# Optimization experiments

Measured on AMD Instinct MI355X. Metric: run time of the kernel, lower is better.

## Reference

```python
import jax, jax.numpy as jnp
import numpy as np

EPS_COS = 1e-8   # F.cosine_similarity eps
EPS_CLAMP = 1e-6 # torch.clamp min on similarities


def setup_inputs() -> dict:
    key = jax.random.key(0)
    k1, = jax.random.split(key, 1)
    N, G, D = 2048, 10, 512
    x = jax.random.normal(k1, (N, G, D), dtype=jnp.float32)
    w = jnp.asarray(10.0, dtype=jnp.float32)  # learnable scale (init_w)
    b = jnp.asarray(-5.0, dtype=jnp.float32)  # learnable bias (init_b)
    return {"x": x, "w": w, "b": b}


def _safe_norm(v, axis=-1, keepdims=True):
    return jnp.maximum(jnp.linalg.norm(v, axis=axis, keepdims=keepdims), EPS_COS)


def reference(x, w, b):
    # x: [N, G, D]  (N speakers, G utterances each, D-dim embeddings)
    N, G, D = x.shape
    sum_x = jnp.sum(x, axis=1)                    # [N, D]
    centroids = sum_x / G                         # [N, D] full centroids
    # exclusion centroid for utterance g of speaker n: mean over the other G-1
    exc = (sum_x[:, None, :] - x) / (G - 1)       # [N, G, D]

    # diagonal: cos(x[n,g], exc_centroid[n,g])
    diag = jnp.sum(x * exc, axis=-1) / (
        _safe_norm(x, keepdims=False) * _safe_norm(exc, keepdims=False)
    )                                             # [N, G]

    # off-diagonal: cos(x[n,g], centroids[m]) for all m
    xn = x / _safe_norm(x)                        # [N, G, D]
    cn = centroids / _safe_norm(centroids)        # [N, D]
    sim = jnp.einsum("ngd,md->ngm", xn, cn)       # [N, G, N]

    # replace m == n entries with the excluded-centroid similarity
    eye = jnp.eye(N, dtype=bool)                  # [N, N]
    sim = jnp.where(eye[:, None, :], diag[:, :, None], sim)
    sim = jnp.maximum(sim, EPS_CLAMP)

    logits = sim * w + b                          # [N, G, N]
    logp = jax.nn.log_softmax(logits, axis=-1)
    n_idx = jnp.arange(N)
    # CE with label = speaker index n, repeated over the G utterances
    nloss = -jnp.mean(logp[n_idx[:, None], jnp.arange(G)[None, :], n_idx[:, None]])

    pred = jnp.argmax(logits, axis=-1)            # [N, G]
    prec1 = jnp.mean((pred == n_idx[:, None]).astype(jnp.float32)) * 100.0
    return nloss, prec1
```

## Files before the change

kernel.cpp:

```cpp
#include <hip/hip_runtime.h>
#include <math.h>

#define NSPK 2048
#define GUT  10
#define DIM  512
#define NG   (NSPK*GUT)

#define BM 256
#define BN 128
#define BK 64
#define NCB (NSPK/BN)
#define NHB (NCB*2)
#define NRB (NG/BM)
#define NKC (DIM/BK)
#define K3B (NG/256)
#define LBUF 24576

typedef __attribute__((ext_vector_type(4))) int int4v;

__device__ inline void gload_lds16(const void* g, void* l) {
  __builtin_amdgcn_global_load_lds(
      (const __attribute__((address_space(1))) void*)g,
      (__attribute__((address_space(3))) void*)l, 16, 0, 0);
}

__device__ __forceinline__ float mergesum(float a, float b, int mask, bool bsel) {
  const float ss = bsel ? a : b;
  const float sk = bsel ? b : a;
  return sk + __shfl_xor(ss, mask);
}
__device__ inline unsigned pack4i8(float a, float b, float c, float d, float qs) {
  const int q0 = (int)rintf(a * qs) & 255, q1 = (int)rintf(b * qs) & 255;
  const int q2 = (int)rintf(c * qs) & 255, q3 = (int)rintf(d * qs) & 255;
  return (unsigned)q0 | ((unsigned)q1 << 8) | ((unsigned)q2 << 16) | ((unsigned)q3 << 24);
}

__global__ __launch_bounds__(256) void k1_prep(const float* __restrict__ x,
    unsigned char* __restrict__ xn8, unsigned char* __restrict__ cn8,
    float* __restrict__ xs, float* __restrict__ cs, float* __restrict__ diag)
{
  const int n = blockIdx.x * 4 + (threadIdx.x >> 6);
  const int l = threadIdx.x & 63;
  const float* xb = x + (size_t)n * GUT * DIM + l * 8;

  float4 xa[GUT], xc[GUT];
#pragma unroll
  for (int g = 0; g < GUT; ++g) {
    xa[g] = *reinterpret_cast<const float4*>(xb + g * DIM);
    xc[g] = *reinterpret_cast<const float4*>(xb + g * DIM + 4);
  }
  float s0=0,s1=0,s2=0,s3=0,s4=0,s5=0,s6=0,s7=0;
#pragma unroll
  for (int g = 0; g < GUT; ++g) {
    s0 += xa[g].x; s1 += xa[g].y; s2 += xa[g].z; s3 += xa[g].w;
    s4 += xc[g].x; s5 += xc[g].y; s6 += xc[g].z; s7 += xc[g].w;
  }
  float P[GUT], D[GUT];
  float mxa = 0.f;
#pragma unroll
  for (int g = 0; g < GUT; ++g) {
    P[g] = xa[g].x*xa[g].x + xa[g].y*xa[g].y + xa[g].z*xa[g].z + xa[g].w*xa[g].w
         + xc[g].x*xc[g].x + xc[g].y*xc[g].y + xc[g].z*xc[g].z + xc[g].w*xc[g].w;
    D[g] = xa[g].x*s0 + xa[g].y*s1 + xa[g].z*s2 + xa[g].w*s3
         + xc[g].x*s4 + xc[g].y*s5 + xc[g].z*s6 + xc[g].w*s7;
    const float m1 = fmaxf(fmaxf(fabsf(xa[g].x), fabsf(xa[g].y)), fmaxf(fabsf(xa[g].z), fabsf(xa[g].w)));
    const float m2 = fmaxf(fmaxf(fabsf(xc[g].x), fabsf(xc[g].y)), fmaxf(fabsf(xc[g].z), fabsf(xc[g].w)));
    mxa = fmaxf(mxa, fmaxf(m1, m2));
  }
  float S = s0*s0+s1*s1+s2*s2+s3*s3+s4*s4+s5*s5+s6*s6+s7*s7;
  float ms = fmaxf(fmaxf(fmaxf(fabsf(s0),fabsf(s1)),fmaxf(fabsf(s2),fabsf(s3))),
                   fmaxf(fmaxf(fabsf(s4),fabsf(s5)),fmaxf(fabsf(s6),fabsf(s7))));

  const bool b0 = l & 1, b1 = l & 2, b2 = l & 4, b3 = l & 8, b4 = l & 16;
  float P01 = mergesum(P[0], P[1], 1, b0);
  float P23 = mergesum(P[2], P[3], 1, b0);
  float P45 = mergesum(P[4], P[5], 1, b0);
  float P67 = mergesum(P[6], P[7], 1, b0);
  float P89 = mergesum(P[8], P[9], 1, b0);
  float D01 = mergesum(D[0], D[1], 1, b0);
  float D23 = mergesum(D[2], D[3], 1, b0);
  float D45 = mergesum(D[4], D[5], 1, b0);
  float D67 = mergesum(D[6], D[7], 1, b0);
  float D89 = mergesum(D[8], D[9], 1, b0);
  S += __shfl_xor(S, 1);
  float PA1 = mergesum(P01, P23, 2, b1);
  float PB1 = mergesum(P45, P67, 2, b1);
  float DA1 = mergesum(D01, D23, 2, b1);
  float DB1 = mergesum(D45, D67, 2, b1);
  P89 += __shfl_xor(P89, 2); D89 += __shfl_xor(D89, 2); S += __shfl_xor(S, 2);
  float PA = mergesum(PA1, PB1, 4, b2);
  float DA = mergesum(DA1, DB1, 4, b2);
  P89 += __shfl_xor(P89, 4); D89 += __shfl_xor(D89, 4); S += __shfl_xor(S, 4);
  float PX = mergesum(PA, P89, 8, b3);
  float DX = mergesum(DA, D89, 8, b3);
  S += __shfl_xor(S, 8);
  float V = mergesum(PX, DX, 16, b4);
  S += __shfl_xor(S, 16);
  V += __shfl_xor(V, 32);
  S += __shfl_xor(S, 32);

#pragma unroll
  for (int m = 1; m < 64; m <<= 1) mxa = fmaxf(mxa, __shfl_xor(mxa, m));
#pragma unroll
  for (int m = 1; m < 64; m <<= 1) ms = fmaxf(ms, __shfl_xor(ms, m));

  const float pdv = __shfl(V, l + 16);

  const float qs = 127.0f / mxa;
#pragma unroll
  for (int g = 0; g < GUT; ++g) {
    uint2 v; v.x = pack4i8(xa[g].x, xa[g].y, xa[g].z, xa[g].w, qs);
             v.y = pack4i8(xc[g].x, xc[g].y, xc[g].z, xc[g].w, qs);
    reinterpret_cast<uint2*>(xn8)[((size_t)n * GUT + g) * 64 + l] = v;
  }
  const float qsc = 127.0f / ms;
  {
    uint2 cp; cp.x = pack4i8(s0, s1, s2, s3, qsc); cp.y = pack4i8(s4, s5, s6, s7, qsc);
    reinterpret_cast<uint2*>(cn8)[n * 64 + l] = cp;
  }

  if (l < GUT) {
    const float psq = V, pd = pdv;
    const float dxe = (pd - psq) * (1.0f / (GUT - 1));
    float ne2 = (S - 2.f * pd + psq) * (1.0f / ((GUT - 1) * (GUT - 1)));
    ne2 = fmaxf(ne2, 0.f);
    const float rn = fmaxf(sqrtf(psq), 1e-8f);
    diag[n * GUT + l] = dxe / (rn * fmaxf(sqrtf(ne2), 1e-8f));
    xs[n * GUT + l] = mxa / (127.0f * rn);
  }
  if (l == 0) {
    const float cnorm  = sqrtf(S) * (1.0f / GUT);
    const float cscale = (1.0f / GUT) / fmaxf(cnorm, 1e-8f);
    cs[n] = cscale * ms * (1.0f / 127.0f);
  }
}

__global__ __launch_bounds__(512, 4) void k2_mfma(
    const unsigned char* __restrict__ xn8, const unsigned char* __restrict__ cn8,
    const float* __restrict__ xs, const float* __restrict__ cs,
    const float* __restrict__ diag, const float* __restrict__ wp,
    const float* __restrict__ bp, float* __restrict__ partial)
{
  __shared__ char ldsb[3 * LBUF];

  const int tid = threadIdx.x;
  const int l = tid & 63, w = tid >> 6;
  const int swz = (blockIdx.x & 7) * (NRB * NCB / 8) + (blockIdx.x >> 3);
  const int rb = swz >> 4, cb = swz & 15;
  const int rowbase = rb * BM, colbase = cb * BN;

  int4v acc1[4][4];
#pragma unroll
  for (int i = 0; i < 4; ++i)
#pragma unroll
    for (int j = 0; j < 4; ++j)
#pragma unroll
      for (int e = 0; e < 4; ++e) acc1[i][j][e] = 0;

  const int sR = l >> 2;
  const int sC16 = (((l & 3) ^ ((l >> 3) & 3)) << 4);

  const int wr = w >> 1, wc = w & 1;
  const int lr = l & 15, lq = l >> 4;
  int aRel[4], bRel[4];
#pragma unroll
  for (int f = 0; f < 4; ++f) {
    aRel[f] = ((wr * 64 + f * 16 + lr) << 6) + ((lq ^ ((lr >> 1) & 3)) << 4);
    bRel[f] = 16384 + ((wc * 64 + f * 16 + lr) << 6) + ((lq ^ ((lr >> 1) & 3)) << 4);
  }

#define STAGE(buf, kcn) do {                                                   \
    char* dst_ = ldsb + (buf) * LBUF;                                          \
    _Pragma("unroll")                                                          \
    for (int q_ = 0; q_ < 3; ++q_) {                                           \
      const int i_ = w * 3 + q_;                                               \
      const bool isA_ = i_ < 16;                                               \
      const int ri_ = isA_ ? i_ : i_ - 16;                                     \
      const unsigned char* src_ = isA_ ? xn8 : cn8;                            \
      const int base_ = isA_ ? rowbase : colbase;                              \
      const size_t go_ = (size_t)(base_ + ri_ * 16 + sR) * DIM + (size_t)(kcn) * BK + sC16; \
      gload_lds16(src_ + go_, dst_ + (isA_ ? 0 : 16384) + ri_ * 1024);         \
    }                                                                          \
  } while (0)

  STAGE(0, 0);
  STAGE(1, 1);

#pragma unroll
  for (int kc = 0; kc < NKC; ++kc) {
    const int cur = kc % 3;
    if (kc + 2 < NKC) {
      STAGE((kc + 2) % 3, kc + 2);
      asm volatile("s_waitcnt vmcnt(6)" ::: "memory");
    } else if (kc + 1 < NKC) {
      asm volatile("s_waitcnt vmcnt(3)" ::: "memory");
    } else {
      asm volatile("s_waitcnt vmcnt(0)" ::: "memory");
    }
    __builtin_amdgcn_s_barrier();

    const char* base = ldsb + cur * LBUF;
    int4v ah[4], bh4[4];
#pragma unroll
    for (int f = 0; f < 4; ++f) {
      ah[f]  = *reinterpret_cast<const int4v*>(base + aRel[f]);
      bh4[f] = *reinterpret_cast<const int4v*>(base + bRel[f]);
    }
    __builtin_amdgcn_s_setprio(1);
#pragma unroll
    for (int mf = 0; mf < 4; ++mf)
#pragma unroll
      for (int nf = 0; nf < 4; ++nf)
        acc1[mf][nf] = __builtin_amdgcn_mfma_i32_16x16x64_i8(ah[mf], bh4[nf], acc1[mf][nf], 0, 0, 0);
    __builtin_amdgcn_s_setprio(0);
  }
#undef STAGE

  const float wv = wp[0], bvb = bp[0];
  const float MFIX = fabsf(wv) + bvb;
  const float L2E = 1.4426950408889634f;
  const float wl2e = wv * L2E, bl2e = (bvb - MFIX) * L2E;
  float xc4[4];
#pragma unroll
  for (int nf = 0; nf < 4; ++nf)
    xc4[nf] = cs[colbase + wc * 64 + nf * 16 + lr];

  float se16[16], mx16[16];
#pragma unroll
  for (int mf = 0; mf < 4; ++mf) {
#pragma unroll
    for (int r = 0; r < 4; ++r) {
      const int p = mf * 4 + r;
      const int row = rowbase + wr * 64 + mf * 16 + lq * 4 + r;
      const float xsr = xs[row];
      const int tcol = row / GUT - colbase;
      const float dval = diag[row];
      float se = 0.f, mxk = -__builtin_inff();
#pragma unroll
      for (int nf = 0; nf < 4; ++nf) {
        const int coll = wc * 64 + nf * 16 + lr;
        float s = (xsr * xc4[nf]) * (float)acc1[mf][nf][r];
        s = (coll == tcol) ? dval : s;
        s = fmaxf(s, 1e-6f);
        const float kf = fmaf(s, wl2e, bl2e);
        se += exp2f(kf);
        mxk = fmaxf(mxk, kf);
      }
      se16[p] = se; mx16[p] = mxk;
    }
  }

  float seA[8], mxA[8];
  {
    const bool b = lr & 1;
#pragma unroll
    for (int j = 0; j < 8; ++j) {
      seA[j] = (b ? se16[2*j+1] : se16[2*j]) + __shfl_xor(b ? se16[2*j] : se16[2*j+1], 1);
      mxA[j] = fmaxf(b ? mx16[2*j+1] : mx16[2*j], __shfl_xor(b ? mx16[2*j] : mx16[2*j+1], 1));
    }
  }
  float seB[4], mxB[4];
  {
    const bool b = (lr >> 1) & 1;
#pragma unroll
    for (int j = 0; j < 4; ++j) {
      seB[j] = (b ? seA[2*j+1] : seA[2*j]) + __shfl_xor(b ? seA[2*j] : seA[2*j+1], 2);
      mxB[j] = fmaxf(b ? mxA[2*j+1] : mxA[2*j], __shfl_xor(b ? mxA[2*j] : mxA[2*j+1], 2));
    }
  }
  float seC[2], mxC[2];
  {
    const bool b = (lr >> 2) & 1;
#pragma unroll
    for (int j = 0; j < 2; ++j) {
      seC[j] = (b ? seB[2*j+1] : seB[2*j]) + __shfl_xor(b ? seB[2*j] : seB[2*j+1], 4);
      mxC[j] = fmaxf(b ? mxB[2*j+1] : mxB[2*j], __shfl_xor(b ? mxB[2*j] : mxB[2*j+1], 4));
    }
  }
  float seF, mxF;
  {
    const bool b = (lr >> 3) & 1;
    seF = (b ? seC[1] : seC[0]) + __shfl_xor(b ? seC[0] : seC[1], 8);
    mxF = fmaxf(b ? mxC[1] : mxC[0], __shfl_xor(b ? mxC[0] : mxC[1], 8));
  }
  {
    const int prow = rowbase + wr * 64 + (lr >> 2) * 16 + lq * 4 + (lr & 3);
    float2 slot; slot.x = seF; slot.y = mxF;
    *reinterpret_cast<float2*>(partial + ((size_t)(cb * 2 + wc) * NG + prow) * 2) = slot;
  }
}

__global__ __launch_bounds__(256) void k3_rows(const float* __restrict__ partial,
    const float* __restrict__ diag, const float* __restrict__ wp,
    const float* __restrict__ bp, float* __restrict__ bsum)
{
  const int row = blockIdx.x * 256 + threadIdx.x;
  float se = 0.f, mx = -__builtin_inff();
#pragma unroll
  for (int c = 0; c < NHB; ++c) {
    const float2 v = *reinterpret_cast<const float2*>(partial + ((size_t)c * NG + row) * 2);
    se += v.x;
    mx = fmaxf(mx, v.y);
  }
  const float wv = wp[0], bvb = bp[0];
  const float MFIX = fabsf(wv) + bvb;
  const float L2E = 1.4426950408889634f;
  const float wl2e = wv * L2E, bl2e = (bvb - MFIX) * L2E;
  const float tg = fmaf(fmaxf(diag[row], 1e-6f), wl2e, bl2e);
  float sl = tg * 0.6931471805599453f - logf(se);
  float sc = (tg >= mx) ? 1.0f : 0.0f;
  for (int off = 32; off > 0; off >>= 1) { sl += __shfl_down(sl, off); sc += __shfl_down(sc, off); }
  __shared__ float ra[4], rb2[4];
  const int lane = threadIdx.x & 63, wid = threadIdx.x >> 6;
  if (lane == 0) { ra[wid] = sl; rb2[wid] = sc; }
  __syncthreads();
  if (threadIdx.x == 0) {
    float2 v; v.x = ra[0] + ra[1] + ra[2] + ra[3];
    v.y = rb2[0] + rb2[1] + rb2[2] + rb2[3];
    *reinterpret_cast<float2*>(bsum + blockIdx.x * 2) = v;
  }
}

__global__ __launch_bounds__(128) void k4_reduce(const float* __restrict__ bsum,
    float* __restrict__ out)
{
  const int t = threadIdx.x;
  float sl = 0.f, sc = 0.f;
  if (t < K3B) {
    const float2 v = *reinterpret_cast<const float2*>(bsum + t * 2);
    sl = v.x; sc = v.y;
  }
  for (int off = 32; off > 0; off >>= 1) { sl += __shfl_down(sl, off); sc += __shfl_down(sc, off); }
  __shared__ float ra[2], rb2[2];
  const int lane = t & 63, wid = t >> 6;
  if (lane == 0) { ra[wid] = sl; rb2[wid] = sc; }
  __syncthreads();
  if (t == 0) {
    const float S = ra[0] + ra[1];
    const float C = rb2[0] + rb2[1];
    out[0] = -(S * (1.0f / NG));
    out[1] = C * (100.0f / NG);
  }
}

extern "C" void kernel_launch(void* const* d_in, const int* in_sizes, int n_in,
                              void* d_out, int out_size, void* d_ws, size_t ws_size,
                              hipStream_t stream)
{
  const float* x = (const float*)d_in[0];
  const float* w = (const float*)d_in[1];
  const float* b = (const float*)d_in[2];
  float* out = (float*)d_out;

  char* ws = (char*)d_ws;
  unsigned char* xn8 = (unsigned char*)ws;
  unsigned char* cn8 = (unsigned char*)(ws + (size_t)NG * DIM);
  char* after = ws + (size_t)NG * DIM + (size_t)NSPK * DIM;
  float* xs   = (float*)after;
  float* cs   = xs + NG;
  float* diag = cs + NSPK;
  float* part = diag + NG;
  float* bsum = part + (size_t)NHB * NG * 2;

  hipLaunchKernelGGL(k1_prep, dim3(NSPK / 4), dim3(256), 0, stream,
                     x, xn8, cn8, xs, cs, diag);
  hipLaunchKernelGGL(k2_mfma, dim3(NRB * NCB), dim3(512), 0, stream,
                     xn8, cn8, xs, cs, diag, w, b, part);
  hipLaunchKernelGGL(k3_rows, dim3(K3B), dim3(256), 0, stream, part, diag, w, b, bsum);
  hipLaunchKernelGGL(k4_reduce, dim3(1), dim3(128), 0, stream, bsum, out);
}
```

Baseline: 59.02 us.

## Interleave global-to-LDS prefetch with MFMA phases in int8 GEMM main loop

The K-loop of the int8 similarity GEMM is restructured into four phases per K chunk. Each phase loads one A fragment from LDS, issues one of the next-next chunk's global-to-LDS loads, and runs a 4-MFMA group. Barriers sit between phases, and the vmcnt wait moves to the end of each chunk. The aim is to spread memory issue across the compute and keep register pressure low by holding one A fragment instead of four. In exchange it adds many more s_barrier calls per iteration, which may cost synchronisation overhead.

```diff
diff --git a/kernel.cpp b/kernel.cpp
--- a/kernel.cpp
+++ b/kernel.cpp
@@ -169,52 +169,60 @@
     bRel[f] = 16384 + ((wc * 64 + f * 16 + lr) << 6) + ((lq ^ ((lr >> 1) & 3)) << 4);
   }
 
-#define STAGE(buf, kcn) do {                                                   \
+#define STAGE1(buf, kcn, qq) do {                                              \
     char* dst_ = ldsb + (buf) * LBUF;                                          \
-    _Pragma("unroll")                                                          \
-    for (int q_ = 0; q_ < 3; ++q_) {                                           \
-      const int i_ = w * 3 + q_;                                               \
-      const bool isA_ = i_ < 16;                                               \
-      const int ri_ = isA_ ? i_ : i_ - 16;                                     \
-      const unsigned char* src_ = isA_ ? xn8 : cn8;                            \
-      const int base_ = isA_ ? rowbase : colbase;                              \
-      const size_t go_ = (size_t)(base_ + ri_ * 16 + sR) * DIM + (size_t)(kcn) * BK + sC16; \
-      gload_lds16(src_ + go_, dst_ + (isA_ ? 0 : 16384) + ri_ * 1024);         \
-    }                                                                          \
+    const int i_ = w * 3 + (qq);                                               \
+    const bool isA_ = i_ < 16;                                                 \
+    const int ri_ = isA_ ? i_ : i_ - 16;                                       \
+    const unsigned char* src_ = isA_ ? xn8 : cn8;                              \
+    const int base_ = isA_ ? rowbase : colbase;                                \
+    const size_t go_ = (size_t)(base_ + ri_ * 16 + sR) * DIM + (size_t)(kcn) * BK + sC16; \
+    gload_lds16(src_ + go_, dst_ + (isA_ ? 0 : 16384) + ri_ * 1024);           \
   } while (0)
 
-  STAGE(0, 0);
-  STAGE(1, 1);
+  STAGE1(0, 0, 0); STAGE1(0, 0, 1); STAGE1(0, 0, 2);
+  STAGE1(1, 1, 0); STAGE1(1, 1, 1); STAGE1(1, 1, 2);
+  asm volatile("s_waitcnt vmcnt(3)" ::: "memory");
+  __builtin_amdgcn_s_barrier();
 
 #pragma unroll
   for (int kc = 0; kc < NKC; ++kc) {
-    const int cur = kc % 3;
-    if (kc + 2 < NKC) {
-      STAGE((kc + 2) % 3, kc + 2);
-      asm volatile("s_waitcnt vmcnt(6)" ::: "memory");
-    } else if (kc + 1 < NKC) {
-      asm volatile("s_waitcnt vmcnt(3)" ::: "memory");
-    } else {
-      asm volatile("s_waitcnt vmcnt(0)" ::: "memory");
-    }
+    const char* base = ldsb + (kc % 3) * LBUF;
+    const int nb = (kc + 2) % 3;
+    const bool pf = (kc + 2) < NKC;
+    int4v bh4[4], ah;
+
+    ah = *reinterpret_cast<const int4v*>(base + aRel[0]);
+#pragma unroll
+    for (int f = 0; f < 4; ++f)
+      bh4[f] = *reinterpret_cast<const int4v*>(base + bRel[f]);
+    if (pf) STAGE1(nb, kc + 2, 0);
     __builtin_amdgcn_s_barrier();
-
-    const char* base = ldsb + cur * LBUF;
-    int4v ah[4], bh4[4];
-#pragma unroll
-    for (int f = 0; f < 4; ++f) {
-      ah[f]  = *reinterpret_cast<const int4v*>(base + aRel[f]);
-      bh4[f] = *reinterpret_cast<const int4v*>(base + bRel[f]);
-    }
     __builtin_amdgcn_s_setprio(1);
 #pragma unroll
-    for (int mf = 0; mf < 4; ++mf)
+    for (int nf = 0; nf < 4; ++nf)
+      acc1[0][nf] = __builtin_amdgcn_mfma_i32_16x16x64_i8(ah, bh4[nf], acc1[0][nf], 0, 0, 0);
+    __builtin_amdgcn_s_setprio(0);
+    __builtin_amdgcn_s_barrier();
+
+#pragma unroll
+    for (int q = 1; q < 4; ++q) {
+      ah = *reinterpret_cast<const int4v*>(base + aRel[q]);
+      if (pf && q < 3) STAGE1(nb, kc + 2, q);
+      __builtin_amdgcn_s_barrier();
+      __builtin_amdgcn_s_setprio(1);
 #pragma unroll
       for (int nf = 0; nf < 4; ++nf)
-        acc1[mf][nf] = __builtin_amdgcn_mfma_i32_16x16x64_i8(ah[mf], bh4[nf], acc1[mf][nf], 0, 0, 0);
-    __builtin_amdgcn_s_setprio(0);
-  }
-#undef STAGE
+        acc1[q][nf] = __builtin_amdgcn_mfma_i32_16x16x64_i8(ah, bh4[nf], acc1[q][nf], 0, 0, 0);
+      __builtin_amdgcn_s_setprio(0);
+      if (q == 3 && kc + 1 < NKC) {
+        if (pf) asm volatile("s_waitcnt vmcnt(3)" ::: "memory");
+        else    asm volatile("s_waitcnt vmcnt(0)" ::: "memory");
+      }
+      __builtin_amdgcn_s_barrier();
+    }
+  }
+#undef STAGE1
 
   const float wv = wp[0], bvb = bp[0];
   const float MFIX = fabsf(wv) + bvb;
```

New measurement: 61.09 us. 3.5% more time.
